# Performance work log

Measured on AMD Instinct MI355X. Metric: run time of the kernel, lower is better.

The kernel has to match this reference:

```python
import jax, jax.numpy as jnp
import numpy as np

N, C, E = 4096, 128, 10          # nodes, channels, element types
LMAX = 2
NI = (LMAX + 1) ** 2             # 9 spherical components of node_feats
K = {1: 4, 2: 12, 3: 30}         # number of CG paths per correlation order
DIMS = [2 * L + 1 for L in range(LMAX + 1)]  # output irrep dims [1,3,5]


def setup_inputs() -> dict:
    key = jax.random.key(0)
    ks = iter(jax.random.split(key, 64))
    inp = {}
    inp["node_feats"] = jax.random.normal(next(ks), (N, C, NI), jnp.float32)
    inp["sc"] = jax.random.normal(next(ks), (N, C * sum(DIMS)), jnp.float32)
    z = jax.random.randint(next(ks), (N,), 0, E)
    inp["node_attrs"] = jax.nn.one_hot(z, E, dtype=jnp.float32)
    for L, d in enumerate(DIMS):
        # U tensors: fixed Clebsch-Gordan-structured constants (stand-in values,
        # correct shapes/contraction pattern of MACE's U_matrix buffers).
        inp[f"U3_L{L}"] = jax.random.normal(next(ks), (d, NI, NI, NI, K[3]), jnp.float32) * 0.05
        inp[f"U2_L{L}"] = jax.random.normal(next(ks), (d, NI, NI, K[2]), jnp.float32) * 0.05
        inp[f"U1_L{L}"] = jax.random.normal(next(ks), (d, NI, K[1]), jnp.float32) * 0.05
        # Element-dependent path weights [num_elements, k, channels]
        inp[f"W3_L{L}"] = jax.random.normal(next(ks), (E, K[3], C), jnp.float32) / np.sqrt(K[3])
        inp[f"W2_L{L}"] = jax.random.normal(next(ks), (E, K[2], C), jnp.float32) / np.sqrt(K[2])
        inp[f"W1_L{L}"] = jax.random.normal(next(ks), (E, K[1], C), jnp.float32) / np.sqrt(K[1])
        # o3.Linear channel-mixing weight for this irrep
        inp[f"lin_L{L}"] = jax.random.normal(next(ks), (C, C), jnp.float32)
    return inp


def _contract(x, y, U3, U2, U1, W3, W2, W1):
    """MACE symmetric contraction (correlation=3) for one output irrep.
    x: [b,c,n] node feats, y: [b,e] one-hot element attrs.
    Recursive einsum structure from mace.modules.symmetric_contraction.Contraction."""
    out = jnp.einsum('dijnk,ekc,bcn,be->bcdij', U3, W3, x, y)
    c2 = jnp.einsum('dijk,ekc,be->bcdij', U2, W2, y) + out
    out = jnp.einsum('bcdij,bcj->bcdi', c2, x)
    c1 = jnp.einsum('dik,ekc,be->bcdi', U1, W1, y) + out
    return jnp.einsum('bcdi,bci->bcd', c1, x)  # [b,c,d]


def reference(node_feats, sc, node_attrs,
              U3_L0, U2_L0, U1_L0, W3_L0, W2_L0, W1_L0, lin_L0,
              U3_L1, U2_L1, U1_L1, W3_L1, W2_L1, W1_L1, lin_L1,
              U3_L2, U2_L2, U1_L2, W3_L2, W2_L2, W1_L2, lin_L2):
    Us = [(U3_L0, U2_L0, U1_L0), (U3_L1, U2_L1, U1_L1), (U3_L2, U2_L2, U1_L2)]
    Ws = [(W3_L0, W2_L0, W1_L0), (W3_L1, W2_L1, W1_L1), (W3_L2, W2_L2, W1_L2)]
    lins = [lin_L0, lin_L1, lin_L2]
    c = node_feats.shape[1]
    norm = jnp.asarray(1.0 / np.sqrt(c), node_feats.dtype)
    outs = []
    for (u3, u2, u1), (w3, w2, w1), lw in zip(Us, Ws, lins):
        o = _contract(node_feats, node_attrs, u3, u2, u1, w3, w2, w1)  # [b,c,d]
        o = jnp.einsum('bcd,cf->bfd', o, lw) * norm                    # o3.Linear mix
        outs.append(o.reshape(o.shape[0], -1))
    return jnp.concatenate(outs, axis=-1) + sc
```

## Files before the change

### kernel.cpp

```cpp
#include <hip/hip_runtime.h>

#define NNODES 4096
#define NCH    128
#define NE     10
#define PADN   4736
#define NCHUNK 74
#define TSTRIDE 2048
#define DGSTRIDE 672


struct MTab { unsigned short v[220]; };
static constexpr MTab make_mtab() {
    MTab t{};
    int m = 0;
    for (int i = 0; i < 9; ++i) {
        t.v[m++] = (unsigned short)((1 << 12) | (i << 8) | (i << 4) | i);
        for (int j = i; j < 9; ++j) {
            t.v[m++] = (unsigned short)((2 << 12) | (i << 8) | (j << 4) | j);
            for (int n = j; n < 9; ++n)
                t.v[m++] = (unsigned short)((3 << 12) | (i << 8) | (j << 4) | n);
        }
    }
    return t;
}
__constant__ MTab c_mtab = make_mtab();

__global__ __launch_bounds__(1024) void k_prep(
    const float* __restrict__ attrs,
    const float* __restrict__ U3_0, const float* __restrict__ U3_1, const float* __restrict__ U3_2,
    const float* __restrict__ W3_0, const float* __restrict__ W3_1, const float* __restrict__ W3_2,
    const float* __restrict__ U2_0, const float* __restrict__ U2_1, const float* __restrict__ U2_2,
    const float* __restrict__ W2_0, const float* __restrict__ W2_1, const float* __restrict__ W2_2,
    const float* __restrict__ U1_0, const float* __restrict__ U1_1, const float* __restrict__ U1_2,
    const float* __restrict__ W1_0, const float* __restrict__ W1_1, const float* __restrict__ W1_2,
    int* __restrict__ list, int* __restrict__ chunkinfo,
    float* __restrict__ wcat, float* __restrict__ Usym)
{
    int bid = blockIdx.x, t = threadIdx.x;
    if (bid == 0) {
        __shared__ int hist[NE], cur[NE], base[NE + 1], cbase[NE + 1];
        if (t < NE) { hist[t] = 0; cur[t] = 0; }
        __syncthreads();
        int mye[4];
#pragma unroll
        for (int k = 0; k < 4; ++k) {
            int b = k * 1024 + t;
            const float* y = attrs + (size_t)b * NE;
            int e = 0;
#pragma unroll
            for (int u = 0; u < NE; ++u) if (y[u] > 0.5f) e = u;
            mye[k] = e;
            atomicAdd(&hist[e], 1);
        }
        for (int i = t; i < PADN; i += 1024) list[i] = -1;
        __syncthreads();
        if (t == 0) {
            int off = 0, goff = 0;
            for (int e = 0; e < NE; ++e) {
                base[e] = off; cbase[e] = goff;
                int nc = (hist[e] + 63) >> 6;
                off += nc * 64; goff += nc;
            }
            base[NE] = off; cbase[NE] = goff;
        }
        __syncthreads();
        if (t < 80) {
            int info = -1;
            if (t < cbase[NE]) {
                int e = 0;
                while (!(t >= cbase[e] && t < cbase[e + 1])) ++e;
                int k = t - cbase[e];
                int valid = hist[e] - k * 64; if (valid > 64) valid = 64;
                info = (base[e] + k * 64) | (valid << 16) | (e << 24);
            }
            chunkinfo[t] = info;
        }
#pragma unroll
        for (int k = 0; k < 4; ++k) {
            int e = mye[k];
            int pos = atomicAdd(&cur[e], 1);
            list[base[e] + pos] = k * 1024 + t;
        }
    } else if (bid <= 10) {
        int e = bid - 1;
        for (int it = t; it < 128 * 48; it += 1024) {
            int c = it & 127, k = it >> 7;
            float v = 0.0f;
            if (k < 4)       v = W1_0[0], v = ((k < 4) ? ((e < NE) ? 0.0f : 0.0f) : 0.0f), v = 0.0f;
            if (k < 4) {
                const float* W1 = W1_0;
                v = 0.0f;
            }
            (void)v;
            break;
        }
        for (int it = t; it < 128 * 48; it += 1024) {
            int c = it & 127, k = it >> 7;
            break;
        }
        int e2 = bid - 1;
#pragma unroll 1
        for (int L = 0; L < 3; ++L) {
            const float* W1 = (L == 0) ? W1_0 : (L == 1) ? W1_1 : W1_2;
            const float* W2 = (L == 0) ? W2_0 : (L == 1) ? W2_1 : W2_2;
            const float* W3 = (L == 0) ? W3_0 : (L == 1) ? W3_1 : W3_2;
            for (int it = t; it < 128 * 48; it += 1024) {
                int c = it & 127, k = it >> 7;
                float v = 0.0f;
                if (k < 4)       v = W1[((size_t)e2 * 4 + k) * 128 + c];
                else if (k < 16) v = W2[((size_t)e2 * 12 + (k - 4)) * 128 + c];
                else if (k < 46) v = W3[((size_t)e2 * 30 + (k - 16)) * 128 + c];
                wcat[(((size_t)L * NE + e2) * 128 + c) * 48 + k] = v;
            }
        }
    } else {
        int D = bid - 11;
        const float *U3, *U2, *U1; int dloc;
        if (D == 0)      { U3 = U3_0; U2 = U2_0; U1 = U1_0; dloc = 0; }
        else if (D < 4)  { U3 = U3_1; U2 = U2_1; U1 = U1_1; dloc = D - 1; }
        else             { U3 = U3_2; U2 = U2_2; U1 = U1_2; dloc = D - 4; }
        for (int it = t; it < 219 * 48; it += 1024) {
            int m = it / 48, k = it - m * 48;
            unsigned mv = c_mtab.v[m];
            int kind = mv >> 12, i = (mv >> 8) & 15, j = (mv >> 4) & 15, n = mv & 15;
            float v = 0.0f;
            if (kind == 1) {
                if (k < 4) v = U1[(size_t)(dloc * 9 + i) * 4 + k];
            } else if (kind == 2) {
                if (k >= 4 && k < 16) {
                    int kk = k - 4;
                    v = U2[(size_t)(dloc * 81 + i * 9 + j) * 12 + kk];
                    if (i != j) v += U2[(size_t)(dloc * 81 + j * 9 + i) * 12 + kk];
                }
            } else {
                if (k >= 16 && k < 46) {
                    int kk = k - 16;
                    v = U3[((size_t)dloc * 729 + i * 81 + j * 9 + n) * 30 + kk];
                    if (i == j) {
                        if (j != n)
                            v += U3[((size_t)dloc * 729 + i * 81 + n * 9 + i) * 30 + kk]
                               + U3[((size_t)dloc * 729 + n * 81 + i * 9 + i) * 30 + kk];
                    } else if (j == n) {
                        v += U3[((size_t)dloc * 729 + j * 81 + i * 9 + j) * 30 + kk]
                           + U3[((size_t)dloc * 729 + j * 81 + j * 9 + i) * 30 + kk];
                    } else {
                        v += U3[((size_t)dloc * 729 + i * 81 + n * 9 + j) * 30 + kk]
                           + U3[((size_t)dloc * 729 + j * 81 + i * 9 + n) * 30 + kk]
                           + U3[((size_t)dloc * 729 + j * 81 + n * 9 + i) * 30 + kk]
                           + U3[((size_t)dloc * 729 + n * 81 + i * 9 + j) * 30 + kk]
                           + U3[((size_t)dloc * 729 + n * 81 + j * 9 + i) * 30 + kk];
                    }
                }
            }
            Usym[((size_t)D * 219 + m) * 48 + k] = v;
        }
    }
}

__global__ __launch_bounds__(256) void k_gt(
    const float* __restrict__ nf, const int* __restrict__ list,
    const float* __restrict__ wcat, const float* __restrict__ Usym,
    float* __restrict__ xg, float* __restrict__ Sws)
{
    int bid = blockIdx.x, t = threadIdx.x;
    if (bid < 1184) {
        __shared__ __align__(16) float smem[64 * 73];
        __shared__ int lb[64];
        int qb = bid >> 4, ct = bid & 15;
        int c0 = ct * 8;
        if (t < 64) lb[t] = list[qb * 64 + t];
        __syncthreads();
#pragma unroll 1
        for (int k = 0; k < 18; ++k) {
            int idx = k * 256 + t;
            int node = idx / 72, elem = idx - node * 72;
            int nb = lb[node];
            float v = 0.0f;
            if (nb >= 0) v = nf[(size_t)nb * 1152 + c0 * 9 + elem];
            smem[node * 73 + elem] = v;
        }
        __syncthreads();
#pragma unroll 1
        for (int k = 0; k < 18; ++k) {
            int idx = k * 256 + t;
            int node = idx & 63, re = idx >> 6;
            xg[((size_t)(c0 * 9 + re)) * PADN + qb * 64 + node] = smem[node * 73 + re];
        }
    } else {
        int bid2 = bid - 1184;
        int e = bid2 / 12, r = bid2 - e * 12;
        int dg = r >> 2, mq = r & 3;
        int c = t & 127;
        int sub = __builtin_amdgcn_readfirstlane(threadIdx.x >> 7);
        float* outp = Sws + ((size_t)e * NCH + c) * TSTRIDE + dg * DGSTRIDE;
        int m0 = mq * 55 + sub, m1 = mq * 55 + 55; if (m1 > 219) m1 = 219;
#pragma unroll 1
        for (int m = m0; m < m1; m += 2) {
            unsigned mv = c_mtab.v[m];
            int kind = mv >> 12;
#pragma unroll
            for (int dr = 0; dr < 3; ++dr) {
                int D = dg * 3 + dr;
                int L = (D == 0) ? 0 : (D < 4 ? 1 : 2);
                const float* wc = wcat + (((size_t)L * NE + e) * 128 + c) * 48;
                const float* up = Usym + ((size_t)D * 219 + m) * 48;
                float acc = 0.0f;
                if (kind == 1) {
#pragma unroll
                    for (int k = 0; k < 4; ++k) acc = fmaf(up[k], wc[k], acc);
                } else if (kind == 2) {
#pragma unroll
                    for (int k = 4; k < 16; ++k) acc = fmaf(up[k], wc[k], acc);
                } else {
#pragma unroll
                    for (int k = 16; k < 46; ++k) acc = fmaf(up[k], wc[k], acc);
                }
                outp[m * 3 + dr] = acc;
            }
        }
    }
}

__global__ __launch_bounds__(256) void k_main(
    const float* __restrict__ xg, const int* __restrict__ chunkinfo,
    const float* __restrict__ Sws, float* __restrict__ pre)
{
    __shared__ __align__(16) float tabs[4][TSTRIDE];
    int c = blockIdx.x;
    int w = threadIdx.x >> 6, lane = threadIdx.x & 63;
    int g = blockIdx.y * 4 + w;
    int info = __builtin_amdgcn_readfirstlane(chunkinfo[g]);
    if (info == -1) return;
    int beg = info & 0xffff;
    int e = (info >> 24) & 0xff;
    int pos = beg + lane;

    {
        const float4* src = (const float4*)(Sws + ((size_t)e * NCH + c) * TSTRIDE);
        float4* dst = (float4*)tabs[w];
#pragma unroll
        for (int k = 0; k < 8; ++k)
            dst[lane + k * 64] = src[lane + k * 64];
    }

    const float* xq = xg + (size_t)c * 9 * PADN;
    float* prep     = pre + (size_t)c * 9 * PADN;

    float x[9];
#pragma unroll
    for (int n = 0; n < 9; ++n) x[n] = xq[(size_t)n * PADN + pos];

#pragma unroll 1
    for (int dg = 0; dg < 3; ++dg) {
        const float* s = tabs[w] + dg * DGSTRIDE;
        float a3[3] = {0.0f, 0.0f, 0.0f};
        int p = 0;
#pragma unroll
        for (int i = 0; i < 9; ++i) {
            float a2[3];
#pragma unroll
            for (int d = 0; d < 3; ++d) a2[d] = s[p + d];
            p += 3;
#pragma unroll
            for (int j = i; j < 9; ++j) {
                float a1[3];
#pragma unroll
                for (int d = 0; d < 3; ++d) a1[d] = s[p + d];
                p += 3;
#pragma unroll
                for (int n = j; n < 9; ++n) {
#pragma unroll
                    for (int d = 0; d < 3; ++d) a1[d] = fmaf(s[p + d], x[n], a1[d]);
                    p += 3;
                }
#pragma unroll
                for (int d = 0; d < 3; ++d) a2[d] = fmaf(a1[d], x[j], a2[d]);
            }
#pragma unroll
            for (int d = 0; d < 3; ++d) a3[d] = fmaf(a2[d], x[i], a3[d]);
        }
#pragma unroll
        for (int d = 0; d < 3; ++d)
            prep[(size_t)(dg * 3 + d) * PADN + pos] = a3[d];
    }
}

__global__ __launch_bounds__(256) void k_mix(
    const float* __restrict__ pre, const int* __restrict__ chunkinfo,
    const float* __restrict__ lin0, const float* __restrict__ lin1,
    const float* __restrict__ lin2, float* __restrict__ mixed)
{
    __shared__ __align__(16) float pt[128 * 64];
    int bid = blockIdx.x;
    int nt = bid >> 1;
    int fbase = (bid & 1) * 64;
    int n0 = nt * 64;
    int D = nt / NCHUNK;
    int g = nt - D * NCHUNK;
    if (chunkinfo[g] == -1) return;
    const float* lin = (D == 0) ? lin0 : (D < 4 ? lin1 : lin2);
    int t = threadIdx.x;

    {
        int q4 = (t & 15) * 4;
        int cb = t >> 4;
#pragma unroll
        for (int k = 0; k < 8; ++k) {
            int c = cb + k * 16;
            float4 v = *(const float4*)&pre[(size_t)c * 9 * PADN + n0 + q4];
            *(float4*)&pt[c * 64 + q4] = v;
        }
    }
    __syncthreads();

    int tq = t & 63;
    int f0 = fbase + __builtin_amdgcn_readfirstlane(t >> 6) * 16;
    float acc[16];
#pragma unroll
    for (int f = 0; f < 16; ++f) acc[f] = 0.0f;

#pragma unroll 4
    for (int c = 0; c < 128; ++c) {
        float pv = pt[c * 64 + tq];
        const float* lr = lin + c * 128 + f0;
#pragma unroll
        for (int f = 0; f < 16; ++f)
            acc[f] = fmaf(pv, lr[f], acc[f]);
    }

    const float nrm = 0.08838834764831845f;
#pragma unroll
    for (int f = 0; f < 16; ++f)
        mixed[(size_t)(f0 + f) * 9 * PADN + n0 + tq] = acc[f] * nrm;
}

__global__ __launch_bounds__(256) void k_out(
    const float* __restrict__ mixed, const int* __restrict__ list,
    const int* __restrict__ chunkinfo, const float* __restrict__ sc,
    float* __restrict__ out)
{
    __shared__ float tr[64 * 73];
    int fc = blockIdx.x, g = blockIdx.y;
    if (chunkinfo[g] == -1) return;
    int t = threadIdx.x;
    int fbase = fc * 8;
    int tf = t >> 6, tq = t & 63;

#pragma unroll
    for (int k = 0; k < 18; ++k) {
        int row = k * 4 + tf;
        int f = row / 9, D = row - f * 9;
        float v = mixed[((size_t)(fbase + f) * 9 + D) * PADN + g * 64 + tq];
        tr[tq * 73 + row] = v;
    }
    __syncthreads();

#pragma unroll 1
    for (int k = 0; k < 18; ++k) {
        int idx = k * 256 + t;
        int node = idx / 72, col = idx - node * 72;
        int b = list[g * 64 + node];
        if (b < 0) continue;
        int row, gcol;
        if (col < 8)       { row = col * 9;                       gcol = fbase + col; }
        else if (col < 32) { int u = col - 8;  int f = u / 3, dl = u - f * 3;
                             row = f * 9 + 1 + dl;                gcol = 128 + fbase * 3 + u; }
        else               { int u = col - 32; int f = u / 5, dl = u - f * 5;
                             row = f * 9 + 4 + dl;                gcol = 512 + fbase * 5 + u; }
        out[(size_t)b * 1152 + gcol] = tr[node * 73 + row] + sc[(size_t)b * 1152 + gcol];
    }
}

extern "C" void kernel_launch(void* const* d_in, const int* in_sizes, int n_in,
                              void* d_out, int out_size, void* d_ws, size_t ws_size,
                              hipStream_t stream)
{
    const float* nf    = (const float*)d_in[0];
    const float* sc    = (const float*)d_in[1];
    const float* attrs = (const float*)d_in[2];
    const float *U3s[3], *U2s[3], *U1s[3], *W3s[3], *W2s[3], *W1s[3], *lins[3];
    for (int L = 0; L < 3; ++L) {
        const int o = 3 + 7 * L;
        U3s[L]  = (const float*)d_in[o + 0];
        U2s[L]  = (const float*)d_in[o + 1];
        U1s[L]  = (const float*)d_in[o + 2];
        W3s[L]  = (const float*)d_in[o + 3];
        W2s[L]  = (const float*)d_in[o + 4];
        W1s[L]  = (const float*)d_in[o + 5];
        lins[L] = (const float*)d_in[o + 6];
    }

    float* wsf     = (float*)d_ws;
    int* chunkinfo = (int*)d_ws;
    int* list      = chunkinfo + 80;
    float* Sws   = wsf + 4864;
    float* pre   = Sws + (size_t)NE * NCH * TSTRIDE;
    float* xg    = pre + (size_t)NCH * 9 * PADN;
    float* wcat  = xg + (size_t)NCH * 9 * PADN;
    float* Usym  = wcat + (size_t)3 * NE * NCH * 48;
    float* mixed = xg;

    k_prep<<<20, 1024, 0, stream>>>(attrs,
                                    U3s[0], U3s[1], U3s[2], W3s[0], W3s[1], W3s[2],
                                    U2s[0], U2s[1], U2s[2], W2s[0], W2s[1], W2s[2],
                                    U1s[0], U1s[1], U1s[2], W1s[0], W1s[1], W1s[2],
                                    list, chunkinfo, wcat, Usym);
    k_gt<<<1304, 256, 0, stream>>>(nf, list, wcat, Usym, xg, Sws);
    k_main<<<dim3(128, 19), 256, 0, stream>>>(xg, chunkinfo, Sws, pre);
    k_mix<<<1332, 256, 0, stream>>>(pre, chunkinfo, lins[0], lins[1], lins[2], mixed);
    k_out<<<dim3(16, NCHUNK), 256, 0, stream>>>(mixed, list, chunkinfo, sc, (float*)d_out);
}
```

Before: 287.5 us.

## Drop node-feature transpose pass; gather features directly in main kernel

Removes the gather-and-transpose stage that wrote a channel-major copy of node features (xg). k_main now reads each node's 9 components straight from node_feats through the sorted list. The per-element table build moves into its own small kernel, which keeps the W weights in registers and uses a k-major wcat layout for coalesced loads. This saves a full write and reread of the features, but the direct gather reads 9 contiguous floats per lane at a stride of 128*9 floats, so coalescing is poor. Dead loops left in k_prep are also deleted.

```diff
diff --git a/kernel.cpp b/kernel.cpp
--- a/kernel.cpp
+++ b/kernel.cpp
@@ -83,34 +83,18 @@
         }
     } else if (bid <= 10) {
         int e = bid - 1;
-        for (int it = t; it < 128 * 48; it += 1024) {
-            int c = it & 127, k = it >> 7;
-            float v = 0.0f;
-            if (k < 4)       v = W1_0[0], v = ((k < 4) ? ((e < NE) ? 0.0f : 0.0f) : 0.0f), v = 0.0f;
-            if (k < 4) {
-                const float* W1 = W1_0;
-                v = 0.0f;
-            }
-            (void)v;
-            break;
-        }
-        for (int it = t; it < 128 * 48; it += 1024) {
-            int c = it & 127, k = it >> 7;
-            break;
-        }
-        int e2 = bid - 1;
 #pragma unroll 1
         for (int L = 0; L < 3; ++L) {
             const float* W1 = (L == 0) ? W1_0 : (L == 1) ? W1_1 : W1_2;
             const float* W2 = (L == 0) ? W2_0 : (L == 1) ? W2_1 : W2_2;
             const float* W3 = (L == 0) ? W3_0 : (L == 1) ? W3_1 : W3_2;
-            for (int it = t; it < 128 * 48; it += 1024) {
+            for (int it = t; it < 48 * 128; it += 1024) {
                 int c = it & 127, k = it >> 7;
                 float v = 0.0f;
-                if (k < 4)       v = W1[((size_t)e2 * 4 + k) * 128 + c];
-                else if (k < 16) v = W2[((size_t)e2 * 12 + (k - 4)) * 128 + c];
-                else if (k < 46) v = W3[((size_t)e2 * 30 + (k - 16)) * 128 + c];
-                wcat[(((size_t)L * NE + e2) * 128 + c) * 48 + k] = v;
+                if (k < 4)       v = W1[((size_t)e * 4 + k) * 128 + c];
+                else if (k < 16) v = W2[((size_t)e * 12 + (k - 4)) * 128 + c];
+                else if (k < 46) v = W3[((size_t)e * 30 + (k - 16)) * 128 + c];
+                wcat[(((size_t)L * NE + e) * 48 + k) * 128 + c] = v;
             }
         }
     } else {
@@ -157,73 +141,69 @@
     }
 }
 
-__global__ __launch_bounds__(256) void k_gt(
+__global__ __launch_bounds__(256) void k_tab(
+    const float* __restrict__ wcat, const float* __restrict__ Usym,
+    float* __restrict__ Sws)
+{
+    int bid = blockIdx.x;
+    int e = bid / 12, r = bid - e * 12;
+    int dg = r >> 2, mq = r & 3;
+    int t = threadIdx.x;
+    int c = t & 127;
+    int sub = __builtin_amdgcn_readfirstlane(t >> 7);
+    int D0 = dg * 3;
+    int LA = (D0 == 0) ? 0 : (D0 < 4 ? 1 : 2);
+    int LB = (D0 + 1 < 4) ? 1 : 2;
+
+    float wcA[48], wcB[48];
+#pragma unroll
+    for (int k = 0; k < 48; ++k) {
+        wcA[k] = wcat[(((size_t)LA * NE + e) * 48 + k) * 128 + c];
+        wcB[k] = wcat[(((size_t)LB * NE + e) * 48 + k) * 128 + c];
+    }
+
+    float* outp = Sws + ((size_t)e * NCH + c) * TSTRIDE + dg * DGSTRIDE;
+    int m1 = mq * 55 + 55; if (m1 > 219) m1 = 219;
+#pragma unroll 1
+    for (int m = mq * 55 + sub; m < m1; m += 2) {
+        unsigned mv = c_mtab.v[m];
+        int kind = mv >> 12;
+        const float* up0 = Usym + ((size_t)D0 * 219 + m) * 48;
+        const float* up1 = up0 + 219 * 48;
+        const float* up2 = up1 + 219 * 48;
+        float a0 = 0.0f, a1 = 0.0f, a2 = 0.0f;
+        if (kind == 1) {
+#pragma unroll
+            for (int k = 0; k < 4; ++k) {
+                a0 = fmaf(up0[k], wcA[k], a0);
+                a1 = fmaf(up1[k], wcB[k], a1);
+                a2 = fmaf(up2[k], wcB[k], a2);
+            }
+        } else if (kind == 2) {
+#pragma unroll
+            for (int k = 4; k < 16; ++k) {
+                a0 = fmaf(up0[k], wcA[k], a0);
+                a1 = fmaf(up1[k], wcB[k], a1);
+                a2 = fmaf(up2[k], wcB[k], a2);
+            }
+        } else {
+#pragma unroll
+            for (int k = 16; k < 46; ++k) {
+                a0 = fmaf(up0[k], wcA[k], a0);
+                a1 = fmaf(up1[k], wcB[k], a1);
+                a2 = fmaf(up2[k], wcB[k], a2);
+            }
+        }
+        outp[m * 3 + 0] = a0;
+        outp[m * 3 + 1] = a1;
+        outp[m * 3 + 2] = a2;
+    }
+}
+
+__global__ __launch_bounds__(256) void k_main(
     const float* __restrict__ nf, const int* __restrict__ list,
-    const float* __restrict__ wcat, const float* __restrict__ Usym,
-    float* __restrict__ xg, float* __restrict__ Sws)
-{
-    int bid = blockIdx.x, t = threadIdx.x;
-    if (bid < 1184) {
-        __shared__ __align__(16) float smem[64 * 73];
-        __shared__ int lb[64];
-        int qb = bid >> 4, ct = bid & 15;
-        int c0 = ct * 8;
-        if (t < 64) lb[t] = list[qb * 64 + t];
-        __syncthreads();
-#pragma unroll 1
-        for (int k = 0; k < 18; ++k) {
-            int idx = k * 256 + t;
-            int node = idx / 72, elem = idx - node * 72;
-            int nb = lb[node];
-            float v = 0.0f;
-            if (nb >= 0) v = nf[(size_t)nb * 1152 + c0 * 9 + elem];
-            smem[node * 73 + elem] = v;
-        }
-        __syncthreads();
-#pragma unroll 1
-        for (int k = 0; k < 18; ++k) {
-            int idx = k * 256 + t;
-            int node = idx & 63, re = idx >> 6;
-            xg[((size_t)(c0 * 9 + re)) * PADN + qb * 64 + node] = smem[node * 73 + re];
-        }
-    } else {
-        int bid2 = bid - 1184;
-        int e = bid2 / 12, r = bid2 - e * 12;
-        int dg = r >> 2, mq = r & 3;
-        int c = t & 127;
-        int sub = __builtin_amdgcn_readfirstlane(threadIdx.x >> 7);
-        float* outp = Sws + ((size_t)e * NCH + c) * TSTRIDE + dg * DGSTRIDE;
-        int m0 = mq * 55 + sub, m1 = mq * 55 + 55; if (m1 > 219) m1 = 219;
-#pragma unroll 1
-        for (int m = m0; m < m1; m += 2) {
-            unsigned mv = c_mtab.v[m];
-            int kind = mv >> 12;
-#pragma unroll
-            for (int dr = 0; dr < 3; ++dr) {
-                int D = dg * 3 + dr;
-                int L = (D == 0) ? 0 : (D < 4 ? 1 : 2);
-                const float* wc = wcat + (((size_t)L * NE + e) * 128 + c) * 48;
-                const float* up = Usym + ((size_t)D * 219 + m) * 48;
-                float acc = 0.0f;
-                if (kind == 1) {
-#pragma unroll
-                    for (int k = 0; k < 4; ++k) acc = fmaf(up[k], wc[k], acc);
-                } else if (kind == 2) {
-#pragma unroll
-                    for (int k = 4; k < 16; ++k) acc = fmaf(up[k], wc[k], acc);
-                } else {
-#pragma unroll
-                    for (int k = 16; k < 46; ++k) acc = fmaf(up[k], wc[k], acc);
-                }
-                outp[m * 3 + dr] = acc;
-            }
-        }
-    }
-}
-
-__global__ __launch_bounds__(256) void k_main(
-    const float* __restrict__ xg, const int* __restrict__ chunkinfo,
-    const float* __restrict__ Sws, float* __restrict__ pre)
+    const int* __restrict__ chunkinfo, const float* __restrict__ Sws,
+    float* __restrict__ pre)
 {
     __shared__ __align__(16) float tabs[4][TSTRIDE];
     int c = blockIdx.x;
@@ -234,6 +214,14 @@
     int beg = info & 0xffff;
     int e = (info >> 24) & 0xff;
     int pos = beg + lane;
+    int b = list[pos];
+
+    float x[9];
+    {
+        const float* xp = nf + ((size_t)(b < 0 ? 0 : b) * 128 + c) * 9;
+#pragma unroll
+        for (int n = 0; n < 9; ++n) x[n] = (b >= 0) ? xp[n] : 0.0f;
+    }
 
     {
         const float4* src = (const float4*)(Sws + ((size_t)e * NCH + c) * TSTRIDE);
@@ -243,12 +231,7 @@
             dst[lane + k * 64] = src[lane + k * 64];
     }
 
-    const float* xq = xg + (size_t)c * 9 * PADN;
-    float* prep     = pre + (size_t)c * 9 * PADN;
-
-    float x[9];
-#pragma unroll
-    for (int n = 0; n < 9; ++n) x[n] = xq[(size_t)n * PADN + pos];
+    float* prep = pre + (size_t)c * 9 * PADN;
 
 #pragma unroll 1
     for (int dg = 0; dg < 3; ++dg) {
@@ -395,18 +378,17 @@
     int* list      = chunkinfo + 80;
     float* Sws   = wsf + 4864;
     float* pre   = Sws + (size_t)NE * NCH * TSTRIDE;
-    float* xg    = pre + (size_t)NCH * 9 * PADN;
-    float* wcat  = xg + (size_t)NCH * 9 * PADN;
-    float* Usym  = wcat + (size_t)3 * NE * NCH * 48;
-    float* mixed = xg;
+    float* mixed = pre + (size_t)NCH * 9 * PADN;
+    float* wcat  = mixed + (size_t)NCH * 9 * PADN;
+    float* Usym  = wcat + (size_t)3 * NE * 48 * 128;
 
     k_prep<<<20, 1024, 0, stream>>>(attrs,
                                     U3s[0], U3s[1], U3s[2], W3s[0], W3s[1], W3s[2],
                                     U2s[0], U2s[1], U2s[2], W2s[0], W2s[1], W2s[2],
                                     U1s[0], U1s[1], U1s[2], W1s[0], W1s[1], W1s[2],
                                     list, chunkinfo, wcat, Usym);
-    k_gt<<<1304, 256, 0, stream>>>(nf, list, wcat, Usym, xg, Sws);
-    k_main<<<dim3(128, 19), 256, 0, stream>>>(xg, chunkinfo, Sws, pre);
+    k_tab<<<120, 256, 0, stream>>>(wcat, Usym, Sws);
+    k_main<<<dim3(128, 19), 256, 0, stream>>>(nf, list, chunkinfo, Sws, pre);
     k_mix<<<1332, 256, 0, stream>>>(pre, chunkinfo, lins[0], lins[1], lins[2], mixed);
     k_out<<<dim3(16, NCHUNK), 256, 0, stream>>>(mixed, list, chunkinfo, sc, (float*)d_out);
 }
```

After: 260.1 us. -9.5%, faster.
